# Performance work log

Hardware: AMD Instinct MI355X
Metric: run time of the kernel (lower is better)

## Reference

```python
import jax, jax.numpy as jnp
import numpy as np
from jax import lax

B, H, W, CIN = 1, 100, 100, 1024
A = 9                      # len(anc_sizes)*len(anc_ratios)
C_BOT = 512
PRE, POST, IOU_THR = 6000, 300, 0.7   # eval path (training=False)


def setup_inputs() -> dict:
    key = jax.random.key(0)
    ks = jax.random.split(key, 9)
    std = 0.01  # RandomNormal(0, 0.01) as in the keras module
    feats = jax.random.normal(ks[0], (B, H, W, CIN), jnp.float32)
    centers = jax.random.uniform(ks[1], (B, H, W, A, 2), jnp.float32)
    wh = jax.random.uniform(ks[2], (B, H, W, A, 2), jnp.float32, minval=0.05, maxval=0.3)
    ancs = jnp.concatenate([centers, wh], axis=-1)          # ccwh, normalized
    ancs_valid = jnp.ones((B, H, W, A), jnp.float32)
    W_b = jax.random.normal(ks[3], (CIN, C_BOT), jnp.float32) * std
    b_b = jnp.zeros((C_BOT,), jnp.float32)
    W_cls = jax.random.normal(ks[4], (C_BOT, A), jnp.float32) * std
    b_cls = jnp.zeros((A,), jnp.float32)
    W_reg = jax.random.normal(ks[5], (C_BOT, A * 4), jnp.float32) * std
    b_reg = jnp.zeros((A * 4,), jnp.float32)
    return dict(feats=feats, ancs=ancs, ancs_valid=ancs_valid,
                W_b=W_b, b_b=b_b, W_cls=W_cls, b_cls=b_cls, W_reg=W_reg, b_reg=b_reg)


def _pairwise_iou(boxes):
    # boxes: [N,4] xyxy
    x1, y1, x2, y2 = boxes[:, 0], boxes[:, 1], boxes[:, 2], boxes[:, 3]
    area = (x2 - x1) * (y2 - y1)                              # [N]
    ix1 = jnp.maximum(x1[:, None], x1[None, :])
    iy1 = jnp.maximum(y1[:, None], y1[None, :])
    ix2 = jnp.minimum(x2[:, None], x2[None, :])
    iy2 = jnp.minimum(y2[:, None], y2[None, :])
    inter = jnp.maximum(ix2 - ix1, 0.0) * jnp.maximum(iy2 - iy1, 0.0)
    union = area[:, None] + area[None, :] - inter
    return inter / jnp.maximum(union, 1e-9)


def _nms_keep(boxes, valid):
    # greedy NMS over score-sorted boxes -> keep mask [N]
    iou = _pairwise_iou(boxes)
    n = boxes.shape[0]

    def step(keep_mask, i):
        suppressed = jnp.any(keep_mask & (iou[i] > IOU_THR))
        k = (~suppressed) & valid[i]
        return keep_mask.at[i].set(k), None

    keep, _ = lax.scan(step, jnp.zeros((n,), bool), jnp.arange(n))
    return keep


def _extract_proposals(cls_pred, reg_pred, ancs):
    grid_w, grid_h = cls_pred.shape[1], cls_pred.shape[2]
    scores = cls_pred.reshape(-1)           # [B*H*W*A]
    offs = reg_pred.reshape(-1, 4)
    anc = ancs.reshape(-1, 4)               # ccwh
    # apply_offsets: standard RPN decode
    xy = anc[:, :2] + offs[:, :2] * anc[:, 2:]
    wh = anc[:, 2:] * jnp.exp(offs[:, 2:])
    boxes = jnp.concatenate([xy - wh / 2, xy + wh / 2], axis=-1)   # ccwh -> xyxy
    boxes = jnp.clip(boxes, 0.0, 1.0)
    sizes = (boxes[:, 2:] - boxes[:, :2]) * jnp.array([grid_w, grid_h], jnp.float32)
    ok = jnp.all(sizes >= 1.0, axis=-1)
    # masked sort replaces boolean filtering (jit-safe); sigmoid scores are > 0,
    # so -1 marks filtered-out proposals
    masked = jnp.where(ok, scores, -1.0)
    top_scores, top_idx = lax.top_k(masked, PRE)     # descending
    top_boxes = boxes[top_idx]
    valid = top_scores > -0.5
    keep = _nms_keep(lax.stop_gradient(top_boxes), valid)
    # first POST kept boxes (in score order), zero-padded to fixed shape
    n = PRE
    prio = jnp.where(keep, jnp.arange(n), n + jnp.arange(n))
    order = jnp.argsort(prio)[:POST]
    out = jnp.where(keep[order][:, None], top_boxes[order], 0.0)
    return out


def reference(feats, ancs, ancs_valid, W_b, b_b, W_cls, b_cls, W_reg, b_reg):
    h = jax.nn.relu(jnp.einsum('bhwc,cd->bhwd', feats, W_b) + b_b)   # 1x1 conv
    cls_pred = jax.nn.sigmoid(jnp.einsum('bhwd,da->bhwa', h, W_cls) + b_cls)
    reg_pred = (jnp.einsum('bhwd,dk->bhwk', h, W_reg) + b_reg).reshape(B, H, W, A, 4)
    proposals = _extract_proposals(cls_pred, reg_pred, ancs)
    return cls_pred, reg_pred, proposals
```

## Files before the change

### kernel.cpp

```cpp
#include <hip/hip_runtime.h>
#include <math.h>

typedef unsigned int U32;
typedef unsigned long long U64;

#define NBOX   90000
#define NPIX   10000
#define KDIM   1024
#define CBOT   512
#define PRE_N  6000
#define POST_N 300
#define NWORD  94
#define MROWS  6016

#define OFF_H       0ULL
#define OFF_BOXES   20480000ULL
#define OFF_KEYS    21920000ULL
#define OFF_MASKT   22280000ULL
#define OFF_SEL     26804032ULL
#define OFF_SBOX    26852032ULL
#define OFF_VALIDW  26948032ULL
#define OFF_KEEPW   26948800ULL
#define OFF_HIST    26949568ULL
#define OFF_CNT     26950592ULL
#define OFF_TIE     26950848ULL
#define WS_NEED     26967232ULL


__global__ __launch_bounds__(256, 4) void k_gemm1(
    const float* __restrict__ A, const float* __restrict__ W,
    const float* __restrict__ bias, float* __restrict__ H,
    U32* __restrict__ hist, U32* __restrict__ cnt, U32* __restrict__ validw32)
{
  int t = threadIdx.x;
  if (blockIdx.x == 0) {
    hist[t] = 0;
    if (t < 64)  cnt[t] = (t == 1) ? (U32)PRE_N : 0u;
    if (t < 188) validw32[t] = 0;
  }
  int bid = blockIdx.x;
  int c = bid & 7;
  int s = bid >> 3;
  int x = s / 10;
  int yy = c * 10 + (s % 10);
  if (yy >= 79) return;
  __shared__ float As[16][132];
  __shared__ float Bs[16][68];
  int m0 = yy * 128, n0 = x * 64;
  int tm = t >> 4, tn = t & 15;
  int ar = t >> 1, ac = (t & 1) << 3;
  int bk = t >> 4, bc = (t & 15) << 2;
  float acc[8][4];
#pragma unroll
  for (int i = 0; i < 8; ++i)
#pragma unroll
    for (int j = 0; j < 4; ++j) acc[i][j] = 0.f;

  int arow = m0 + ar;
  float4 a0 = make_float4(0.f,0.f,0.f,0.f), a1 = a0;
  if (arow < NPIX) {
    a0 = *(const float4*)&A[(size_t)arow * KDIM + ac];
    a1 = *(const float4*)&A[(size_t)arow * KDIM + ac + 4];
  }
  float4 b0 = *(const float4*)&W[(size_t)bk * CBOT + n0 + bc];

  for (int k0 = 0; k0 < KDIM; k0 += 16) {
    __syncthreads();
    As[ac+0][ar] = a0.x; As[ac+1][ar] = a0.y; As[ac+2][ar] = a0.z; As[ac+3][ar] = a0.w;
    As[ac+4][ar] = a1.x; As[ac+5][ar] = a1.y; As[ac+6][ar] = a1.z; As[ac+7][ar] = a1.w;
    *(float4*)&Bs[bk][bc] = b0;
    __syncthreads();
    if (k0 + 16 < KDIM) {
      int kn = k0 + 16;
      if (arow < NPIX) {
        a0 = *(const float4*)&A[(size_t)arow * KDIM + kn + ac];
        a1 = *(const float4*)&A[(size_t)arow * KDIM + kn + ac + 4];
      }
      b0 = *(const float4*)&W[(size_t)(kn + bk) * CBOT + n0 + bc];
    }
#pragma unroll
    for (int kk = 0; kk < 16; ++kk) {
      float4 av0 = *(float4*)&As[kk][tm*8];
      float4 av1 = *(float4*)&As[kk][tm*8+4];
      float4 bv0 = *(float4*)&Bs[kk][tn*4];
      float am[8] = {av0.x,av0.y,av0.z,av0.w,av1.x,av1.y,av1.z,av1.w};
      float bm[4] = {bv0.x,bv0.y,bv0.z,bv0.w};
#pragma unroll
      for (int i = 0; i < 8; ++i)
#pragma unroll
        for (int j = 0; j < 4; ++j)
          acc[i][j] = fmaf(am[i], bm[j], acc[i][j]);
    }
  }
  float4 bb = *(const float4*)&bias[n0 + tn*4];
  float bm[4] = {bb.x, bb.y, bb.z, bb.w};
#pragma unroll
  for (int i = 0; i < 8; ++i) {
    int r = m0 + tm*8 + i;
    if (r < NPIX) {
      float4 o;
      o.x = fmaxf(acc[i][0] + bm[0], 0.f);
      o.y = fmaxf(acc[i][1] + bm[1], 0.f);
      o.z = fmaxf(acc[i][2] + bm[2], 0.f);
      o.w = fmaxf(acc[i][3] + bm[3], 0.f);
      *(float4*)&H[(size_t)r * CBOT + n0 + tn*4] = o;
    }
  }
}

__global__ __launch_bounds__(256) void k_heads(
    const float* __restrict__ H, const float* __restrict__ Wc,
    const float* __restrict__ bc, const float* __restrict__ Wr,
    const float* __restrict__ br, float* __restrict__ outCls,
    float* __restrict__ outReg)
{
  __shared__ float hs[4][516];
  int t = threadIdx.x;
  int p0 = blockIdx.x * 4;
  for (int q = t; q < 512; q += 256) {
    int row = q >> 7, off = (q & 127) << 2;
    *(float4*)&hs[row][off] = *(const float4*)&H[(size_t)(p0 + row) * CBOT + off];
  }
  __syncthreads();
  if (t < 180) {
    int pl = t / 45, c = t % 45;
    const float* wp; int stride; float bval;
    if (c < 9) { wp = Wc + c;       stride = 9;  bval = bc[c]; }
    else       { wp = Wr + (c - 9); stride = 36; bval = br[c - 9]; }
    float s = 0.f;
    const float* hrow = hs[pl];
    for (int k = 0; k < CBOT; k += 4) {
      float4 hv = *(const float4*)&hrow[k];
      s = fmaf(hv.x, wp[(size_t)(k+0)*stride], s);
      s = fmaf(hv.y, wp[(size_t)(k+1)*stride], s);
      s = fmaf(hv.z, wp[(size_t)(k+2)*stride], s);
      s = fmaf(hv.w, wp[(size_t)(k+3)*stride], s);
    }
    s += bval;
    int p = p0 + pl;
    if (c < 9) outCls[(size_t)p*9 + c] = 1.f / (1.f + expf(-s));
    else       outReg[(size_t)p*36 + (c - 9)] = s;
  }
}

__global__ __launch_bounds__(256) void k_decode(
    const float* __restrict__ outCls, const float* __restrict__ outReg,
    const float* __restrict__ ancs, float* __restrict__ boxes,
    U32* __restrict__ keys, U32* __restrict__ hist)
{
  __shared__ U32 lh[256];
  int t = threadIdx.x;
  int tid = blockIdx.x * 256 + t;
  lh[t] = 0;
  __syncthreads();
  if (tid < NBOX) {
    float sc = outCls[tid];
    float4 of = *(const float4*)&outReg[(size_t)tid*4];
    float4 an = *(const float4*)&ancs[(size_t)tid*4];
    float cx = an.x + of.x * an.z;
    float cy = an.y + of.y * an.w;
    float ww = an.z * expf(of.z);
    float hh = an.w * expf(of.w);
    float x1 = fminf(fmaxf(cx - ww * 0.5f, 0.f), 1.f);
    float y1 = fminf(fmaxf(cy - hh * 0.5f, 0.f), 1.f);
    float x2 = fminf(fmaxf(cx + ww * 0.5f, 0.f), 1.f);
    float y2 = fminf(fmaxf(cy + hh * 0.5f, 0.f), 1.f);
    bool ok = ((x2 - x1) * 100.f >= 1.f) && ((y2 - y1) * 100.f >= 1.f);
    float msc = ok ? sc : -1.f;
    U32 u = __float_as_uint(msc);
    U32 key = (u & 0x80000000u) ? ~u : (u | 0x80000000u);
    keys[tid] = key;
    *(float4*)&boxes[(size_t)tid*4] = make_float4(x1, y1, x2, y2);
    atomicAdd(&lh[key >> 24], 1u);
  }
  __syncthreads();
  if (lh[t]) atomicAdd(&hist[t], lh[t]);
}

__global__ __launch_bounds__(256) void k_scan(
    U32* __restrict__ hist, U32* __restrict__ cnt, int level)
{
  __shared__ U32 lh[256];
  int t = threadIdx.x;
  lh[t] = hist[t];
  __syncthreads();
  if (t == 0) {
    U32 target = cnt[1];
    U32 cum = 0;
    int d = 255;
    while (d > 0) {
      U32 hh = lh[d];
      if (cum + hh >= target) break;
      cum += hh; --d;
    }
    cnt[0] |= ((U32)d) << (24 - 8*level);
    cnt[1] = target - cum;
    cnt[2] += cum;
  }
  __syncthreads();
  hist[t] = 0;
}

__global__ __launch_bounds__(256) void k_hist(
    const U32* __restrict__ keys, U32* __restrict__ hist,
    const U32* __restrict__ cnt, int level)
{
  __shared__ U32 lh[256];
  int t = threadIdx.x;
  int tid = blockIdx.x * 256 + t;
  lh[t] = 0;
  __syncthreads();
  if (tid < NBOX) {
    U32 k = keys[tid];
    U32 prefix = cnt[0];
    int shift = 32 - 8*level;
    if ((k >> shift) == (prefix >> shift)) {
      U32 bin = (k >> (24 - 8*level)) & 0xFFu;
      atomicAdd(&lh[bin], 1u);
    }
  }
  __syncthreads();
  if (lh[t]) atomicAdd(&hist[t], lh[t]);
}

__global__ __launch_bounds__(256) void k_compact(
    const U32* __restrict__ keys, U32* __restrict__ cnt,
    U64* __restrict__ sel, U32* __restrict__ tiebuf)
{
  int tid = blockIdx.x * 256 + threadIdx.x;
  if (tid >= NBOX) return;
  U32 k = keys[tid];
  U32 T = cnt[0];
  if (k > T) {
    U32 p = atomicAdd(&cnt[8], 1u);
    sel[p] = ((U64)k << 32) | (U64)(0xFFFFFFFFu - (U32)tid);
  } else if (k == T) {
    U32 p = atomicAdd(&cnt[9], 1u);
    if (p < 4096) tiebuf[p] = (U32)tid;
  }
}

__global__ __launch_bounds__(256) void k_ties(
    U32* __restrict__ cnt, const U32* __restrict__ tiebuf, U64* __restrict__ sel)
{
  __shared__ U32 tb[4096];
  int t = threadIdx.x;
  U32 m = cnt[9]; if (m > 4096u) m = 4096u;
  U32 need = cnt[1];
  U32 cgt  = cnt[2];
  U32 T    = cnt[0];
  for (U32 j = t; j < m; j += 256) tb[j] = tiebuf[j];
  __syncthreads();
  for (U32 x = t; x < m; x += 256) {
    U32 my = tb[x];
    U32 r = 0;
    for (U32 j = 0; j < m; ++j) r += (tb[j] < my) ? 1u : 0u;
    if (r < need) sel[cgt + r] = ((U64)T << 32) | (U64)(0xFFFFFFFFu - my);
  }
}

__global__ __launch_bounds__(256) void k_rank(
    const U64* __restrict__ sel, const float* __restrict__ boxes,
    float* __restrict__ sboxes, U64* __restrict__ validw)
{
  __shared__ U64 ss[PRE_N];
  int t = threadIdx.x;
  for (int j = t; j < PRE_N; j += 256) ss[j] = sel[j];
  __syncthreads();
  int i = blockIdx.x * 256 + t;
  if (i >= PRE_N) return;
  U64 C = ss[i];
  int r = 0;
  for (int j = 0; j < PRE_N; ++j) r += (ss[j] > C) ? 1 : 0;
  U32 key = (U32)(C >> 32);
  U32 idx = 0xFFFFFFFFu - (U32)(C & 0xFFFFFFFFull);
  *(float4*)&sboxes[(size_t)r*4] = *(const float4*)&boxes[(size_t)idx*4];
  if (key & 0x80000000u)
    atomicOr(&validw[r >> 6], 1ull << (r & 63));
}

__global__ __launch_bounds__(256) void k_mask(
    const float* __restrict__ sboxes, U64* __restrict__ maskT)
{
  int cw = blockIdx.x, rg = blockIdx.y;
  if (rg < cw) return;
  int t = threadIdx.x;
  int lane = t & 63, wv = t >> 6;
  int col = cw * 64 + lane;
  int cc = (col < PRE_N) ? col : (PRE_N - 1);
  float4 cb = *(const float4*)&sboxes[(size_t)cc*4];
  float areaC = (cb.z - cb.x) * (cb.w - cb.y);
  bool colok = (col < PRE_N);
  for (int rr = wv; rr < 64; rr += 4) {
    int row = rg * 64 + rr;
    U64 word = 0;
    if (row < PRE_N) {
      float4 rb = *(const float4*)&sboxes[(size_t)row*4];
      float areaR = (rb.z - rb.x) * (rb.w - rb.y);
      float ix1 = fmaxf(rb.x, cb.x), iy1 = fmaxf(rb.y, cb.y);
      float ix2 = fminf(rb.z, cb.z), iy2 = fminf(rb.w, cb.w);
      float inter = fmaxf(ix2 - ix1, 0.f) * fmaxf(iy2 - iy1, 0.f);
      float uni = areaR + areaC - inter;
      float iou = inter / fmaxf(uni, 1e-9f);
      word = __ballot(colok && (iou > 0.7f));
    }
    if (lane == 0) maskT[(size_t)cw * MROWS + row] = word;
  }
}

__global__ __launch_bounds__(512, 1) void k_nms(
    const U64* __restrict__ maskT, const U64* __restrict__ validw,
    U64* __restrict__ keepw)
{
  __shared__ U32 sup[MROWS];
  __shared__ U64 vws[NWORD];
  __shared__ U64 kwsh;
  int t = threadIdx.x;
  int wave = t >> 6, lane = t & 63;
  for (int i = t; i < MROWS; i += 512) sup[i] = 0;
  if (t < NWORD) vws[t] = validw[t];
  U64 low = (lane == 0) ? 0ull : (~0ull >> (64 - lane));
  U64 intra = (wave == 0) ? maskT[lane] : 0ull;
  __syncthreads();
  for (int c = 0; c < NWORD; ++c) {
    const U64* colp = maskT + (size_t)c * MROWS;
    int base = (c + 1) * 64;
    U64 m[12];
#pragma unroll
    for (int q = 0; q < 12; ++q) {
      int i = base + q * 512 + t;
      int ic = (i > MROWS - 1) ? (MROWS - 1) : i;
      m[q] = colp[ic];
    }
    if (wave == 0) {
      U64 vw = vws[c];
      bool alive = (((vw >> lane) & 1ull) != 0ull) && (sup[c * 64 + lane] == 0u);
      U64 aliveW = __ballot(alive);
      bool myconf = alive && ((intra & aliveW & low) != 0ull);
      U64 confW = __ballot(myconf);
      U64 keep = aliveW & ~confW;
      U64 rem = confW;
      while (rem) {
        int b = __ffsll((unsigned long long)rem) - 1;
        rem &= rem - 1;
        U64 Z = __ballot((intra & keep & low) == 0ull);
        if ((Z >> b) & 1ull) keep |= (1ull << b);
      }
      if (lane == 0) { keepw[c] = keep; kwsh = keep; }
      if (c + 1 < NWORD)
        intra = maskT[(size_t)(c + 1) * MROWS + (c + 1) * 64 + lane];
    }
    __syncthreads();
    U64 keep = kwsh;
#pragma unroll
    for (int q = 0; q < 12; ++q) {
      int i = base + q * 512 + t;
      if (i < PRE_N && (m[q] & keep)) sup[i] = 1u;
    }
    __syncthreads();
  }
}

__global__ __launch_bounds__(256) void k_out(
    const U64* __restrict__ keepw, const float* __restrict__ sboxes,
    float* __restrict__ prop)
{
  __shared__ U64 kw[NWORD];
  __shared__ U32 pre[NWORD + 1];
  int t = threadIdx.x;
  if (t < NWORD) kw[t] = keepw[t];
  __syncthreads();
  if (t == 0) {
    U32 s = 0;
    for (int w = 0; w < NWORD; ++w) { pre[w] = s; s += (U32)__popcll(kw[w]); }
    pre[NWORD] = s;
  }
  for (int x = t; x < POST_N * 4; x += 256) prop[x] = 0.f;
  __syncthreads();
  for (int i = t; i < PRE_N; i += 256) {
    int w = i >> 6, b = i & 63;
    if ((kw[w] >> b) & 1ull) {
      U64 lowb = (b == 0) ? 0ull : (~0ull >> (64 - b));
      U32 r = pre[w] + (U32)__popcll(kw[w] & lowb);
      if (r < POST_N)
        *(float4*)&prop[(size_t)r*4] = *(const float4*)&sboxes[(size_t)i*4];
    }
  }
}

extern "C" void kernel_launch(void* const* d_in, const int* in_sizes, int n_in,
                              void* d_out, int out_size, void* d_ws, size_t ws_size,
                              hipStream_t stream)
{
  (void)in_sizes; (void)n_in; (void)out_size;
  if (ws_size < WS_NEED) return;

  const float* feats = (const float*)d_in[0];
  const float* ancs  = (const float*)d_in[1];
  const float* W_b   = (const float*)d_in[3];
  const float* b_b   = (const float*)d_in[4];
  const float* W_cls = (const float*)d_in[5];
  const float* b_cls = (const float*)d_in[6];
  const float* W_reg = (const float*)d_in[7];
  const float* b_reg = (const float*)d_in[8];

  float* out    = (float*)d_out;
  float* outCls = out;
  float* outReg = out + 90000;
  float* prop   = out + 450000;

  char* ws = (char*)d_ws;
  float* H      = (float*)(ws + OFF_H);
  float* boxes  = (float*)(ws + OFF_BOXES);
  U32*   keys   = (U32*)  (ws + OFF_KEYS);
  U64*   maskT  = (U64*)  (ws + OFF_MASKT);
  U64*   sel    = (U64*)  (ws + OFF_SEL);
  float* sboxes = (float*)(ws + OFF_SBOX);
  U64*   validw = (U64*)  (ws + OFF_VALIDW);
  U64*   keepw  = (U64*)  (ws + OFF_KEEPW);
  U32*   hist   = (U32*)  (ws + OFF_HIST);
  U32*   cnt    = (U32*)  (ws + OFF_CNT);
  U32*   tiebuf = (U32*)  (ws + OFF_TIE);

  k_gemm1<<<dim3(640), dim3(256), 0, stream>>>(feats, W_b, b_b, H,
                                               hist, cnt, (U32*)validw);
  k_heads<<<dim3(2500), dim3(256), 0, stream>>>(H, W_cls, b_cls, W_reg, b_reg,
                                                outCls, outReg);
  k_decode<<<dim3(352), dim3(256), 0, stream>>>(outCls, outReg, ancs,
                                                boxes, keys, hist);
  k_scan<<<dim3(1), dim3(256), 0, stream>>>(hist, cnt, 0);
  for (int lv = 1; lv <= 3; ++lv) {
    k_hist<<<dim3(352), dim3(256), 0, stream>>>(keys, hist, cnt, lv);
    k_scan<<<dim3(1), dim3(256), 0, stream>>>(hist, cnt, lv);
  }
  k_compact<<<dim3(352), dim3(256), 0, stream>>>(keys, cnt, sel, tiebuf);
  k_ties<<<dim3(1), dim3(256), 0, stream>>>(cnt, tiebuf, sel);
  k_rank<<<dim3(24), dim3(256), 0, stream>>>(sel, boxes, sboxes, validw);
  k_mask<<<dim3(94, 94), dim3(256), 0, stream>>>(sboxes, maskT);
  k_nms<<<dim3(1), dim3(512), 0, stream>>>(maskT, validw, keepw);
  k_out<<<dim3(1), dim3(256), 0, stream>>>(keepw, sboxes, prop);
}
```

Measured before the change: 530.3 us.

## Fold radix-select scans into histogram/compact kernels and merge output into NMS

Removes the four single-block k_scan launches by keeping one histogram per radix level and having each consumer block redundantly recompute the threshold with a parallel suffix scan. The separate k_out kernel is merged into the tail of k_nms, and k_rank's rank-counting loop reads shared memory with 128-bit vector loads. This cuts serial launches and tiny kernels from the selection pipeline, at the cost of redundant per-block scans (extra syncs and LDS traffic in every block). The tie buffer is also reduced in size.

```diff
diff --git a/kernel.cpp b/kernel.cpp
--- a/kernel.cpp
+++ b/kernel.cpp
@@ -12,6 +12,7 @@
 #define POST_N 300
 #define NWORD  94
 #define MROWS  6016
+#define NTIE   3072
 
 #define OFF_H       0ULL
 #define OFF_BOXES   20480000ULL
@@ -21,21 +22,51 @@
 #define OFF_SBOX    26852032ULL
 #define OFF_VALIDW  26948032ULL
 #define OFF_KEEPW   26948800ULL
-#define OFF_HIST    26949568ULL
 #define OFF_CNT     26950592ULL
-#define OFF_TIE     26950848ULL
+#define OFF_HIST4   26950848ULL
+#define OFF_TIE     26954944ULL
 #define WS_NEED     26967232ULL
 
+
+__device__ __forceinline__ void scan_levels(
+    const U32* __restrict__ histg, int levels, int t,
+    U32* lh, U32* sfx, volatile U32* res)
+{
+  if (t == 0) { res[0] = 0; res[1] = PRE_N; res[2] = 0; }
+  __syncthreads();
+  for (int L = 0; L < levels; ++L) {
+    if (t < 256) { U32 h = histg[L * 256 + t]; lh[t] = h; sfx[t] = h; }
+    if (t == 0) res[3] = 0;
+    __syncthreads();
+    for (int off = 1; off < 256; off <<= 1) {
+      U32 v = 0;
+      if (t < 256) v = sfx[t] + ((t + off < 256) ? sfx[t + off] : 0);
+      __syncthreads();
+      if (t < 256) sfx[t] = v;
+      __syncthreads();
+    }
+    if (t > 0 && t < 256 && sfx[t] >= res[1]) atomicMax((U32*)&res[3], (U32)t);
+    __syncthreads();
+    if (t == 0) {
+      U32 d = res[3];
+      U32 cum = (d < 255) ? sfx[d + 1] : 0;
+      res[0] |= d << (24 - 8 * L);
+      res[1] = res[1] - cum;
+      res[2] += cum;
+    }
+    __syncthreads();
+  }
+}
 
 __global__ __launch_bounds__(256, 4) void k_gemm1(
     const float* __restrict__ A, const float* __restrict__ W,
     const float* __restrict__ bias, float* __restrict__ H,
-    U32* __restrict__ hist, U32* __restrict__ cnt, U32* __restrict__ validw32)
+    U32* __restrict__ hist4, U32* __restrict__ cnt, U32* __restrict__ validw32)
 {
   int t = threadIdx.x;
   if (blockIdx.x == 0) {
-    hist[t] = 0;
-    if (t < 64)  cnt[t] = (t == 1) ? (U32)PRE_N : 0u;
+    hist4[t] = 0; hist4[t + 256] = 0; hist4[t + 512] = 0; hist4[t + 768] = 0;
+    if (t < 64)  cnt[t] = 0u;
     if (t < 188) validw32[t] = 0;
   }
   int bid = blockIdx.x;
@@ -146,7 +177,7 @@
 __global__ __launch_bounds__(256) void k_decode(
     const float* __restrict__ outCls, const float* __restrict__ outReg,
     const float* __restrict__ ancs, float* __restrict__ boxes,
-    U32* __restrict__ keys, U32* __restrict__ hist)
+    U32* __restrict__ keys, U32* __restrict__ hist4)
 {
   __shared__ U32 lh[256];
   int t = threadIdx.x;
@@ -174,45 +205,23 @@
     atomicAdd(&lh[key >> 24], 1u);
   }
   __syncthreads();
-  if (lh[t]) atomicAdd(&hist[t], lh[t]);
-}
-
-__global__ __launch_bounds__(256) void k_scan(
-    U32* __restrict__ hist, U32* __restrict__ cnt, int level)
+  if (lh[t]) atomicAdd(&hist4[t], lh[t]);
+}
+
+__global__ __launch_bounds__(256) void k_hist(
+    const U32* __restrict__ keys, U32* __restrict__ hist4, int level)
 {
   __shared__ U32 lh[256];
-  int t = threadIdx.x;
-  lh[t] = hist[t];
-  __syncthreads();
-  if (t == 0) {
-    U32 target = cnt[1];
-    U32 cum = 0;
-    int d = 255;
-    while (d > 0) {
-      U32 hh = lh[d];
-      if (cum + hh >= target) break;
-      cum += hh; --d;
-    }
-    cnt[0] |= ((U32)d) << (24 - 8*level);
-    cnt[1] = target - cum;
-    cnt[2] += cum;
-  }
-  __syncthreads();
-  hist[t] = 0;
-}
-
-__global__ __launch_bounds__(256) void k_hist(
-    const U32* __restrict__ keys, U32* __restrict__ hist,
-    const U32* __restrict__ cnt, int level)
-{
-  __shared__ U32 lh[256];
-  int t = threadIdx.x;
+  __shared__ U32 sfx[256];
+  __shared__ U32 res[4];
+  int t = threadIdx.x;
+  scan_levels(hist4, level, t, lh, sfx, res);
+  U32 prefix = res[0];
+  lh[t] = 0;
+  __syncthreads();
   int tid = blockIdx.x * 256 + t;
-  lh[t] = 0;
-  __syncthreads();
   if (tid < NBOX) {
     U32 k = keys[tid];
-    U32 prefix = cnt[0];
     int shift = 32 - 8*level;
     if ((k >> shift) == (prefix >> shift)) {
       U32 bin = (k >> (24 - 8*level)) & 0xFFu;
@@ -220,35 +229,45 @@
     }
   }
   __syncthreads();
-  if (lh[t]) atomicAdd(&hist[t], lh[t]);
+  if (lh[t]) atomicAdd(&hist4[level * 256 + t], lh[t]);
 }
 
 __global__ __launch_bounds__(256) void k_compact(
-    const U32* __restrict__ keys, U32* __restrict__ cnt,
-    U64* __restrict__ sel, U32* __restrict__ tiebuf)
-{
-  int tid = blockIdx.x * 256 + threadIdx.x;
+    const U32* __restrict__ keys, const U32* __restrict__ hist4,
+    U32* __restrict__ cnt, U64* __restrict__ sel, U32* __restrict__ tiebuf)
+{
+  __shared__ U32 lh[256];
+  __shared__ U32 sfx[256];
+  __shared__ U32 res[4];
+  int t = threadIdx.x;
+  scan_levels(hist4, 4, t, lh, sfx, res);
+  U32 T = res[0];
+  int tid = blockIdx.x * 256 + t;
   if (tid >= NBOX) return;
   U32 k = keys[tid];
-  U32 T = cnt[0];
   if (k > T) {
     U32 p = atomicAdd(&cnt[8], 1u);
     sel[p] = ((U64)k << 32) | (U64)(0xFFFFFFFFu - (U32)tid);
   } else if (k == T) {
     U32 p = atomicAdd(&cnt[9], 1u);
-    if (p < 4096) tiebuf[p] = (U32)tid;
+    if (p < NTIE) tiebuf[p] = (U32)tid;
   }
 }
 
 __global__ __launch_bounds__(256) void k_ties(
-    U32* __restrict__ cnt, const U32* __restrict__ tiebuf, U64* __restrict__ sel)
-{
-  __shared__ U32 tb[4096];
-  int t = threadIdx.x;
-  U32 m = cnt[9]; if (m > 4096u) m = 4096u;
-  U32 need = cnt[1];
-  U32 cgt  = cnt[2];
-  U32 T    = cnt[0];
+    const U32* __restrict__ hist4, U32* __restrict__ cnt,
+    const U32* __restrict__ tiebuf, U64* __restrict__ sel)
+{
+  __shared__ U32 lh[256];
+  __shared__ U32 sfx[256];
+  __shared__ U32 res[4];
+  __shared__ U32 tb[NTIE];
+  int t = threadIdx.x;
+  scan_levels(hist4, 4, t, lh, sfx, res);
+  U32 T    = res[0];
+  U32 need = res[1];
+  U32 cgt  = res[2];
+  U32 m = cnt[9]; if (m > (U32)NTIE) m = (U32)NTIE;
   for (U32 j = t; j < m; j += 256) tb[j] = tiebuf[j];
   __syncthreads();
   for (U32 x = t; x < m; x += 256) {
@@ -263,7 +282,7 @@
     const U64* __restrict__ sel, const float* __restrict__ boxes,
     float* __restrict__ sboxes, U64* __restrict__ validw)
 {
-  __shared__ U64 ss[PRE_N];
+  __shared__ __align__(16) U64 ss[PRE_N];
   int t = threadIdx.x;
   for (int j = t; j < PRE_N; j += 256) ss[j] = sel[j];
   __syncthreads();
@@ -271,7 +290,11 @@
   if (i >= PRE_N) return;
   U64 C = ss[i];
   int r = 0;
-  for (int j = 0; j < PRE_N; ++j) r += (ss[j] > C) ? 1 : 0;
+  for (int j = 0; j < PRE_N; j += 4) {
+    ulonglong2 v0 = *(const ulonglong2*)&ss[j];
+    ulonglong2 v1 = *(const ulonglong2*)&ss[j + 2];
+    r += (int)(v0.x > C) + (int)(v0.y > C) + (int)(v1.x > C) + (int)(v1.y > C);
+  }
   U32 key = (U32)(C >> 32);
   U32 idx = 0xFFFFFFFFu - (U32)(C & 0xFFFFFFFFull);
   *(float4*)&sboxes[(size_t)r*4] = *(const float4*)&boxes[(size_t)idx*4];
@@ -310,10 +333,12 @@
 
 __global__ __launch_bounds__(512, 1) void k_nms(
     const U64* __restrict__ maskT, const U64* __restrict__ validw,
-    U64* __restrict__ keepw)
+    const float* __restrict__ sboxes, float* __restrict__ prop)
 {
   __shared__ U32 sup[MROWS];
   __shared__ U64 vws[NWORD];
+  __shared__ U64 kwS[NWORD];
+  __shared__ U32 pre[NWORD + 1];
   __shared__ U64 kwsh;
   int t = threadIdx.x;
   int wave = t >> 6, lane = t & 63;
@@ -346,7 +371,7 @@
         U64 Z = __ballot((intra & keep & low) == 0ull);
         if ((Z >> b) & 1ull) keep |= (1ull << b);
       }
-      if (lane == 0) { keepw[c] = keep; kwsh = keep; }
+      if (lane == 0) { kwS[c] = keep; kwsh = keep; }
       if (c + 1 < NWORD)
         intra = maskT[(size_t)(c + 1) * MROWS + (c + 1) * 64 + lane];
     }
@@ -359,29 +384,18 @@
     }
     __syncthreads();
   }
-}
-
-__global__ __launch_bounds__(256) void k_out(
-    const U64* __restrict__ keepw, const float* __restrict__ sboxes,
-    float* __restrict__ prop)
-{
-  __shared__ U64 kw[NWORD];
-  __shared__ U32 pre[NWORD + 1];
-  int t = threadIdx.x;
-  if (t < NWORD) kw[t] = keepw[t];
-  __syncthreads();
   if (t == 0) {
     U32 s = 0;
-    for (int w = 0; w < NWORD; ++w) { pre[w] = s; s += (U32)__popcll(kw[w]); }
+    for (int w = 0; w < NWORD; ++w) { pre[w] = s; s += (U32)__popcll(kwS[w]); }
     pre[NWORD] = s;
   }
-  for (int x = t; x < POST_N * 4; x += 256) prop[x] = 0.f;
-  __syncthreads();
-  for (int i = t; i < PRE_N; i += 256) {
+  for (int x = t; x < POST_N * 4; x += 512) prop[x] = 0.f;
+  __syncthreads();
+  for (int i = t; i < PRE_N; i += 512) {
     int w = i >> 6, b = i & 63;
-    if ((kw[w] >> b) & 1ull) {
+    if ((kwS[w] >> b) & 1ull) {
       U64 lowb = (b == 0) ? 0ull : (~0ull >> (64 - b));
-      U32 r = pre[w] + (U32)__popcll(kw[w] & lowb);
+      U32 r = pre[w] + (U32)__popcll(kwS[w] & lowb);
       if (r < POST_N)
         *(float4*)&prop[(size_t)r*4] = *(const float4*)&sboxes[(size_t)i*4];
     }
@@ -417,26 +431,21 @@
   U64*   sel    = (U64*)  (ws + OFF_SEL);
   float* sboxes = (float*)(ws + OFF_SBOX);
   U64*   validw = (U64*)  (ws + OFF_VALIDW);
-  U64*   keepw  = (U64*)  (ws + OFF_KEEPW);
-  U32*   hist   = (U32*)  (ws + OFF_HIST);
   U32*   cnt    = (U32*)  (ws + OFF_CNT);
+  U32*   hist4  = (U32*)  (ws + OFF_HIST4);
   U32*   tiebuf = (U32*)  (ws + OFF_TIE);
 
   k_gemm1<<<dim3(640), dim3(256), 0, stream>>>(feats, W_b, b_b, H,
-                                               hist, cnt, (U32*)validw);
+                                               hist4, cnt, (U32*)validw);
   k_heads<<<dim3(2500), dim3(256), 0, stream>>>(H, W_cls, b_cls, W_reg, b_reg,
                                                 outCls, outReg);
   k_decode<<<dim3(352), dim3(256), 0, stream>>>(outCls, outReg, ancs,
-                                                boxes, keys, hist);
-  k_scan<<<dim3(1), dim3(256), 0, stream>>>(hist, cnt, 0);
-  for (int lv = 1; lv <= 3; ++lv) {
-    k_hist<<<dim3(352), dim3(256), 0, stream>>>(keys, hist, cnt, lv);
-    k_scan<<<dim3(1), dim3(256), 0, stream>>>(hist, cnt, lv);
-  }
-  k_compact<<<dim3(352), dim3(256), 0, stream>>>(keys, cnt, sel, tiebuf);
-  k_ties<<<dim3(1), dim3(256), 0, stream>>>(cnt, tiebuf, sel);
+                                                boxes, keys, hist4);
+  for (int lv = 1; lv <= 3; ++lv)
+    k_hist<<<dim3(352), dim3(256), 0, stream>>>(keys, hist4, lv);
+  k_compact<<<dim3(352), dim3(256), 0, stream>>>(keys, hist4, cnt, sel, tiebuf);
+  k_ties<<<dim3(1), dim3(256), 0, stream>>>(hist4, cnt, tiebuf, sel);
   k_rank<<<dim3(24), dim3(256), 0, stream>>>(sel, boxes, sboxes, validw);
   k_mask<<<dim3(94, 94), dim3(256), 0, stream>>>(sboxes, maskT);
-  k_nms<<<dim3(1), dim3(512), 0, stream>>>(maskT, validw, keepw);
-  k_out<<<dim3(1), dim3(256), 0, stream>>>(keepw, sboxes, prop);
-}
+  k_nms<<<dim3(1), dim3(512), 0, stream>>>(maskT, validw, sboxes, prop);
+}
```

Result: no change. 526.8 us (-0.7%).
